# Kernel optimization log

Measured on AMD Instinct MI355X. Metric: run time of the kernel, lower is better.

Reference implementation:

```python
import jax, jax.numpy as jnp
import numpy as np

B, IN_UNITS, C, U, K = 32, 16, 8192, 32, 16
NUM_ITERS = 3


def setup_inputs() -> dict:
    key = jax.random.key(0)
    k1, k2 = jax.random.split(key)
    x = jax.random.normal(k1, (B, IN_UNITS, C), dtype=jnp.float32)
    # W corresponds to the torch parameter of shape (1, C, U, K, IN_UNITS), leading 1 dropped
    W = jax.random.normal(k2, (C, U, K, IN_UNITS), dtype=jnp.float32)
    return {"x": x, "W": W}


def reference(x, W):
    batch = x.shape[0]
    # u_hat[b,c,u,k] = sum_i W[c,u,k,i] * x[b,i,c]   (torch: W @ x after transpose/stack)
    u_hat = jnp.einsum('cuki,bic->bcuk', W, x)
    b_ij = jnp.zeros((C, U), dtype=x.dtype)
    v = None
    for _ in range(NUM_ITERS):
        c_ij = jax.nn.softmax(b_ij, axis=0)            # softmax over in_channels (dim=1 in torch)
        s = jnp.einsum('cu,bcuk->buk', c_ij, u_hat)    # weighted sum over channels
        # squash: note the original sums over dim=2 of (B,1,U,K,1) == the num_units axis
        mag_sq = jnp.sum(s ** 2, axis=1, keepdims=True)  # (B,1,K)
        mag = jnp.sqrt(mag_sq)
        v = mag_sq / (1.0 + mag_sq) * (s / mag)          # (B,U,K)
        # agreement: mean over batch of <u_hat, v>
        a = jnp.einsum('bcuk,buk->cu', u_hat, v) / batch
        b_ij = b_ij + a
    return v[..., None]  # matches torch output (B, num_units, unit_size, 1)
```

## Files before the change

kernel.cpp:

```cpp
#include <hip/hip_runtime.h>

#define CC   8192
#define UU   32
#define KK   16
#define BB   32
#define INU  16
#define UK   512
#define CPB  32
#define NBLK 256

__global__ __launch_bounds__(512, 2) void fused_pass(
    const float* __restrict__ x, const float* __restrict__ W,
    const float* __restrict__ v_in, float* __restrict__ b_io,
    float* __restrict__ S, float* __restrict__ Z)
{
    __shared__ float xs[16 * 516];

    const int t   = threadIdx.x;
    const int bid = blockIdx.x;
    const int c0  = bid * CPB;
    const int u   = t >> 4;
    const int k   = t & 15;

    float v[BB], Sl[BB], uh[BB];
#pragma unroll
    for (int b = 0; b < BB; ++b) { v[b] = v_in[b * UK + t]; Sl[b] = 0.f; }
    float zloc = 0.f;

    float4 w0, w1, w2, w3;
    {
        const float4* p = (const float4*)(W + ((size_t)c0 * UK + t) * INU);
        w0 = p[0]; w1 = p[1]; w2 = p[2]; w3 = p[3];
    }

    for (int cc = 0; cc < CPB; ++cc) {
        if ((cc & 15) == 0) {
            __syncthreads();
            const int cbase = c0 + (cc & ~15);
            for (int j = 0; j < 16; ++j) {
                int idx = j * 512 + t;
                int ccl = idx & 15;
                int bi  = idx >> 4;
                xs[ccl * 516 + bi] = x[bi * CC + cbase + ccl];
            }
            __syncthreads();
        }

        float4 n0, n1, n2, n3;
        const bool have_next = (cc + 1 < CPB);
        if (have_next) {
            const float4* p = (const float4*)(W + ((size_t)(c0 + cc + 1) * UK + t) * INU);
            n0 = p[0]; n1 = p[1]; n2 = p[2]; n3 = p[3];
        }

        const float* xrow = &xs[(cc & 15) * 516];
        float ap = 0.f;
#pragma unroll
        for (int b = 0; b < BB; ++b) {
            const float4* xr = (const float4*)(xrow + b * INU);
            float4 x0 = xr[0], x1 = xr[1], x2 = xr[2], x3 = xr[3];
            float h;
            h = w0.x * x0.x;
            h = fmaf(w0.y, x0.y, h); h = fmaf(w0.z, x0.z, h); h = fmaf(w0.w, x0.w, h);
            h = fmaf(w1.x, x1.x, h); h = fmaf(w1.y, x1.y, h);
            h = fmaf(w1.z, x1.z, h); h = fmaf(w1.w, x1.w, h);
            h = fmaf(w2.x, x2.x, h); h = fmaf(w2.y, x2.y, h);
            h = fmaf(w2.z, x2.z, h); h = fmaf(w2.w, x2.w, h);
            h = fmaf(w3.x, x3.x, h); h = fmaf(w3.y, x3.y, h);
            h = fmaf(w3.z, x3.z, h); h = fmaf(w3.w, x3.w, h);
            uh[b] = h;
            ap = fmaf(h, v[b], ap);
        }

        ap += __shfl_xor(ap, 8);
        ap += __shfl_xor(ap, 4);
        ap += __shfl_xor(ap, 2);
        ap += __shfl_xor(ap, 1);

        const int c = c0 + cc;
        float bnew = b_io[c * UU + u] + ap * (1.0f / (float)BB);
        float e = __expf(bnew);
        zloc += e;
        if (k == 0) b_io[c * UU + u] = bnew;

#pragma unroll
        for (int b = 0; b < BB; ++b) Sl[b] = fmaf(e, uh[b], Sl[b]);

        if (have_next) { w0 = n0; w1 = n1; w2 = n2; w3 = n3; }
    }

#pragma unroll
    for (int b = 0; b < BB; ++b) atomicAdd(S + b * UK + t, Sl[b]);
    if (k == 0) atomicAdd(Z + u, zloc);
}

__global__ void squash_k(const float* __restrict__ S, const float* __restrict__ Z,
                         float* __restrict__ vout)
{
    __shared__ float z_sh[UU];
    __shared__ float s2_sh[UK];
    __shared__ float mag_sh[KK];

    const int b = blockIdx.x;
    const int t = threadIdx.x;

    if (t < UU) z_sh[t] = Z[t];
    float ssum = S[b * UK + t];
    __syncthreads();

    float s = ssum / z_sh[t >> 4];
    s2_sh[t] = s * s;
    __syncthreads();

    if (t < KK) {
        float m = 0.f;
        for (int uu = 0; uu < UU; ++uu) m += s2_sh[uu * KK + t];
        mag_sh[t] = m;
    }
    __syncthreads();

    float msq = mag_sh[t & 15];
    float out = (msq / (1.0f + msq)) * s / sqrtf(msq);
    vout[b * UK + t] = out;
}

extern "C" void kernel_launch(void* const* d_in, const int* in_sizes, int n_in,
                              void* d_out, int out_size, void* d_ws, size_t ws_size,
                              hipStream_t stream)
{
    const float* x = (const float*)d_in[0];
    const float* W = (const float*)d_in[1];
    float* out = (float*)d_out;

    char* ws = (char*)d_ws;
    float* S   = (float*)(ws);
    float* Z   = (float*)(ws + 65536);
    float* vb  = (float*)(ws + 65536 + 256);
    float* bio = (float*)(ws + 65536 + 256 + 65536);

    hipMemsetAsync(vb,  0, BB * UK * 4, stream);
    hipMemsetAsync(bio, 0, CC * UU * 4, stream);

    for (int pass = 0; pass < 3; ++pass) {
        hipMemsetAsync(S, 0, BB * UK * 4, stream);
        hipMemsetAsync(Z, 0, UU * 4, stream);
        fused_pass<<<NBLK, 512, 0, stream>>>(x, W, vb, bio, S, Z);
        float* vo = (pass == 2) ? out : vb;
        squash_k<<<BB, UK, 0, stream>>>(S, Z, vo);
    }
}
```

Measured before the change: 707.1 us.

## Pre-transpose x and stream it through scalar loads instead of LDS staging

Adds a transpose kernel that lays x out as [C][B*IN] so every wave reads the same 16-float row. The main pass then fetches those rows with s_load_dwordx16 into SGPRs, double-buffered, and drops the LDS staging and its barriers. It also halves channels per block to double the grid, raises the occupancy hint, and replaces the per-pass memsets with one upfront memset over per-pass S/Z buffers. The old LDS kernel is kept as a fallback when the workspace is too small. Inline asm waitcnt after every body may serialize latency, and the fallback path adds code.

Measured after the change: 1.006 ms. 1.42x slower.

```diff
diff --git a/kernel.cpp b/kernel.cpp
--- a/kernel.cpp
+++ b/kernel.cpp
@@ -6,16 +6,53 @@
 #define BB   32
 #define INU  16
 #define UK   512
-#define CPB  32
-#define NBLK 256
-
-__global__ __launch_bounds__(512, 2) void fused_pass(
-    const float* __restrict__ x, const float* __restrict__ W,
+#define CPB  16
+#define NBLK 512
+
+typedef __attribute__((ext_vector_type(16))) float f32x16;
+
+__global__ __launch_bounds__(256) void transpose_x(
+    const float* __restrict__ x, float* __restrict__ xT)
+{
+    __shared__ float tile[64][65];
+    const int bc = blockIdx.x & 127;
+    const int bb = blockIdx.x >> 7;
+    const int c0 = bc * 64, bi0 = bb * 64;
+    const int tx = threadIdx.x & 63, ty = threadIdx.x >> 6;
+#pragma unroll
+    for (int j = 0; j < 64; j += 4)
+        tile[ty + j][tx] = x[(size_t)(bi0 + ty + j) * CC + (c0 + tx)];
+    __syncthreads();
+#pragma unroll
+    for (int j = 0; j < 64; j += 4)
+        xT[(size_t)(c0 + ty + j) * (BB * INU) + (bi0 + tx)] = tile[tx][ty + j];
+}
+
+#define SBODY(XC, XN, B, NP)                                                  \
+    asm volatile("s_load_dwordx16 %0, %1, 0" : "=s"(XN) : "s"(NP));           \
+    {                                                                         \
+        float h0 = w0.x * XC[0];                                              \
+        float h1 = w0.z * XC[2];                                              \
+        float h2 = w1.x * XC[4];                                              \
+        float h3 = w1.z * XC[6];                                              \
+        h0 = fmaf(w0.y, XC[1],  h0);  h1 = fmaf(w0.w, XC[3],  h1);            \
+        h2 = fmaf(w1.y, XC[5],  h2);  h3 = fmaf(w1.w, XC[7],  h3);            \
+        h0 = fmaf(w2.x, XC[8],  h0);  h1 = fmaf(w2.z, XC[10], h1);            \
+        h2 = fmaf(w3.x, XC[12], h2);  h3 = fmaf(w3.z, XC[14], h3);            \
+        h0 = fmaf(w2.y, XC[9],  h0);  h1 = fmaf(w2.w, XC[11], h1);            \
+        h2 = fmaf(w3.y, XC[13], h2);  h3 = fmaf(w3.w, XC[15], h3);            \
+        float hs = (h0 + h1) + (h2 + h3);                                     \
+        uh[B] = hs;                                                           \
+        ap = fmaf(hs, v[B], ap);                                              \
+    }                                                                         \
+    asm volatile("s_waitcnt lgkmcnt(0)" : "+s"(XN));                          \
+    __builtin_amdgcn_sched_barrier(0);
+
+__global__ __launch_bounds__(512, 4) void fused_pass(
+    const float* __restrict__ W, const float* __restrict__ xT,
     const float* __restrict__ v_in, float* __restrict__ b_io,
     float* __restrict__ S, float* __restrict__ Z)
 {
-    __shared__ float xs[16 * 516];
-
     const int t   = threadIdx.x;
     const int bid = blockIdx.x;
     const int c0  = bid * CPB;
@@ -33,7 +70,81 @@
         w0 = p[0]; w1 = p[1]; w2 = p[2]; w3 = p[3];
     }
 
+    f32x16 xa, xb;
+    {
+        const float* p0 = xT + (size_t)c0 * (BB * INU);
+        asm volatile("s_load_dwordx16 %0, %1, 0" : "=s"(xa) : "s"(p0));
+        asm volatile("s_waitcnt lgkmcnt(0)" : "+s"(xa));
+        __builtin_amdgcn_sched_barrier(0);
+    }
+
     for (int cc = 0; cc < CPB; ++cc) {
+        float4 n0, n1, n2, n3;
+        const bool have_next = (cc + 1 < CPB);
+        if (have_next) {
+            const float4* p = (const float4*)(W + ((size_t)(c0 + cc + 1) * UK + t) * INU);
+            n0 = p[0]; n1 = p[1]; n2 = p[2]; n3 = p[3];
+        }
+
+        const float* xrow  = xT + (size_t)(c0 + cc) * (BB * INU);
+        const float* xnext = have_next ? (xrow + BB * INU) : xrow;
+
+        float ap = 0.f;
+#pragma unroll
+        for (int b = 0; b < BB; b += 2) {
+            const float* np0 = xrow + (size_t)(b + 1) * INU;
+            SBODY(xa, xb, b, np0)
+            const float* np1 = (b + 2 < BB) ? (xrow + (size_t)(b + 2) * INU) : xnext;
+            SBODY(xb, xa, b + 1, np1)
+        }
+
+        ap += __shfl_xor(ap, 8);
+        ap += __shfl_xor(ap, 4);
+        ap += __shfl_xor(ap, 2);
+        ap += __shfl_xor(ap, 1);
+
+        const int c = c0 + cc;
+        float bnew = b_io[c * UU + u] + ap * (1.0f / (float)BB);
+        float e = __expf(bnew);
+        zloc += e;
+        if (k == 0) b_io[c * UU + u] = bnew;
+
+#pragma unroll
+        for (int b = 0; b < BB; ++b) Sl[b] = fmaf(e, uh[b], Sl[b]);
+
+        if (have_next) { w0 = n0; w1 = n1; w2 = n2; w3 = n3; }
+    }
+
+#pragma unroll
+    for (int b = 0; b < BB; ++b) atomicAdd(S + b * UK + t, Sl[b]);
+    if (k == 0) atomicAdd(Z + u, zloc);
+}
+
+__global__ __launch_bounds__(512, 2) void fused_pass_lds(
+    const float* __restrict__ x, const float* __restrict__ W,
+    const float* __restrict__ v_in, float* __restrict__ b_io,
+    float* __restrict__ S, float* __restrict__ Z)
+{
+    __shared__ float xs[16 * 516];
+
+    const int t   = threadIdx.x;
+    const int bid = blockIdx.x;
+    const int c0  = bid * 32;
+    const int u   = t >> 4;
+    const int k   = t & 15;
+
+    float v[BB], Sl[BB], uh[BB];
+#pragma unroll
+    for (int b = 0; b < BB; ++b) { v[b] = v_in[b * UK + t]; Sl[b] = 0.f; }
+    float zloc = 0.f;
+
+    float4 w0, w1, w2, w3;
+    {
+        const float4* p = (const float4*)(W + ((size_t)c0 * UK + t) * INU);
+        w0 = p[0]; w1 = p[1]; w2 = p[2]; w3 = p[3];
+    }
+
+    for (int cc = 0; cc < 32; ++cc) {
         if ((cc & 15) == 0) {
             __syncthreads();
             const int cbase = c0 + (cc & ~15);
@@ -47,7 +158,7 @@
         }
 
         float4 n0, n1, n2, n3;
-        const bool have_next = (cc + 1 < CPB);
+        const bool have_next = (cc + 1 < 32);
         if (have_next) {
             const float4* p = (const float4*)(W + ((size_t)(c0 + cc + 1) * UK + t) * INU);
             n0 = p[0]; n1 = p[1]; n2 = p[2]; n3 = p[3];
@@ -133,19 +244,42 @@
     float* out = (float*)d_out;
 
     char* ws = (char*)d_ws;
-    float* S   = (float*)(ws);
-    float* Z   = (float*)(ws + 65536);
-    float* vb  = (float*)(ws + 65536 + 256);
-    float* bio = (float*)(ws + 65536 + 256 + 65536);
-
-    hipMemsetAsync(vb,  0, BB * UK * 4, stream);
-    hipMemsetAsync(bio, 0, CC * UU * 4, stream);
-
-    for (int pass = 0; pass < 3; ++pass) {
-        hipMemsetAsync(S, 0, BB * UK * 4, stream);
-        hipMemsetAsync(Z, 0, UU * 4, stream);
-        fused_pass<<<NBLK, 512, 0, stream>>>(x, W, vb, bio, S, Z);
-        float* vo = (pass == 2) ? out : vb;
-        squash_k<<<BB, UK, 0, stream>>>(S, Z, vo);
-    }
-}
+
+    const size_t XT_OFF = 0x140400;
+    const size_t NEED   = XT_OFF + (size_t)CC * BB * INU * 4;
+
+    if (ws_size >= NEED) {
+        float* S3  = (float*)(ws);
+        float* Z3  = (float*)(ws + 0x30000);
+        float* vb  = (float*)(ws + 0x30200);
+        float* bio = (float*)(ws + 0x40200);
+        float* xT  = (float*)(ws + XT_OFF);
+
+        hipMemsetAsync(ws, 0, 0x140200, stream);
+        transpose_x<<<1024, 256, 0, stream>>>(x, xT);
+
+        for (int pass = 0; pass < 3; ++pass) {
+            float* S = S3 + (size_t)pass * (BB * UK);
+            float* Z =3 > 0 ? (Z3 + (size_t)pass * 32) : Z3;
+            fused_pass<<<NBLK, 512, 0, stream>>>(W, xT, vb, bio, S, Z);
+            float* vo = (pass == 2) ? out : vb;
+            squash_k<<<BB, UK, 0, stream>>>(S, Z, vo);
+        }
+    } else {
+        float* S   = (float*)(ws);
+        float* Z   = (float*)(ws + 65536);
+        float* vb  = (float*)(ws + 65536 + 256);
+        float* bio = (float*)(ws + 65536 + 256 + 65536);
+
+        hipMemsetAsync(vb,  0, BB * UK * 4, stream);
+        hipMemsetAsync(bio, 0, CC * UU * 4, stream);
+
+        for (int pass = 0; pass < 3; ++pass) {
+            hipMemsetAsync(S, 0, BB * UK * 4, stream);
+            hipMemsetAsync(Z, 0, UU * 4, stream);
+            fused_pass_lds<<<256, 512, 0, stream>>>(x, W, vb, bio, S, Z);
+            float* vo = (pass == 2) ? out : vb;
+            squash_k<<<BB, UK, 0, stream>>>(S, Z, vo);
+        }
+    }
+}
```

## Compute u_hat with split-bf16 MFMA and pre-transposed x

Applied to the files above, without the earlier changes.

Adds a transpose kernel that lays x out as (C, B*IN) once, then replaces the scalar FMA u_hat computation with bf16 MFMA 16x16x32 instructions. Each fp32 value is split into high and low bf16 parts so three products approximate fp32 accuracy. Per-pass S/Z buffers are zeroed with one memset up front to cut launch overhead. The MFMA path drops the LDS staging of x and uses wave-wide shuffle reductions; the old path is kept as a fallback when the workspace is too small.

New measurement: 811.8 us. 1.15x slower.

```diff
diff --git a/kernel.cpp b/kernel.cpp
--- a/kernel.cpp
+++ b/kernel.cpp
@@ -9,7 +9,186 @@
 #define CPB  32
 #define NBLK 256
 
-__global__ __launch_bounds__(512, 2) void fused_pass(
+typedef __attribute__((ext_vector_type(4))) float  f32x4;
+typedef __attribute__((ext_vector_type(8))) __bf16 bf16x8;
+
+__global__ __launch_bounds__(256) void transpose_x(
+    const float* __restrict__ x, float* __restrict__ xT)
+{
+    __shared__ float tile[64][65];
+    const int bc = blockIdx.x & 127;
+    const int bb = blockIdx.x >> 7;
+    const int c0 = bc * 64, bi0 = bb * 64;
+    const int tx = threadIdx.x & 63, ty = threadIdx.x >> 6;
+#pragma unroll
+    for (int j = 0; j < 64; j += 4)
+        tile[ty + j][tx] = x[(size_t)(bi0 + ty + j) * CC + (c0 + tx)];
+    __syncthreads();
+#pragma unroll
+    for (int j = 0; j < 64; j += 4)
+        xT[(size_t)(c0 + ty + j) * (BB * INU) + (bi0 + tx)] = tile[tx][ty + j];
+}
+
+__device__ inline void split4(f32x4 f, __bf16 h[4], __bf16 l[4])
+{
+#pragma unroll
+    for (int i = 0; i < 4; ++i) {
+        __bf16 hh = (__bf16)f[i];
+        h[i] = hh;
+        l[i] = (__bf16)(f[i] - (float)hh);
+    }
+}
+
+__device__ inline bf16x8 pack8(const __bf16 a[4], const __bf16 b[4])
+{
+    bf16x8 r;
+    r[0] = a[0]; r[1] = a[1]; r[2] = a[2]; r[3] = a[3];
+    r[4] = b[0]; r[5] = b[1]; r[6] = b[2]; r[7] = b[3];
+    return r;
+}
+
+__global__ __launch_bounds__(512, 2) void fused_mfma(
+    const float* __restrict__ W, const float* __restrict__ xT,
+    const float* __restrict__ v_in, float* __restrict__ b_io,
+    float* __restrict__ S, float* __restrict__ Z)
+{
+    const int tid  = threadIdx.x;
+    const int w    = tid >> 6;
+    const int lane = tid & 63;
+    const int col  = lane & 15;
+    const int g    = lane >> 4;
+    const int c0   = blockIdx.x * CPB;
+    const int u0   = w * 4;
+    const int loff = col * 16 + g * 4;
+
+    f32x4 vf[4][2], Sl[4][2];
+#pragma unroll
+    for (int uu = 0; uu < 4; ++uu)
+#pragma unroll
+        for (int bt = 0; bt < 2; ++bt) {
+            const int b = bt * 16 + col;
+#pragma unroll
+            for (int r = 0; r < 4; ++r) {
+                vf[uu][bt][r] = v_in[(size_t)b * UK + (u0 + uu) * KK + g * 4 + r];
+                Sl[uu][bt][r] = 0.f;
+            }
+        }
+    float zl[4] = {0.f, 0.f, 0.f, 0.f};
+
+    f32x4 wf[4], xf[2], bio;
+    {
+        const float* wb = W + ((size_t)c0 * UU + u0) * (KK * INU) + loff;
+#pragma unroll
+        for (int uu = 0; uu < 4; ++uu) wf[uu] = *(const f32x4*)(wb + uu * 256);
+        const float* xb = xT + (size_t)c0 * (BB * INU) + loff;
+        xf[0] = *(const f32x4*)(xb);
+        xf[1] = *(const f32x4*)(xb + 256);
+        bio   = *(const f32x4*)(b_io + (size_t)c0 * UU + u0);
+    }
+
+    const __bf16 zb = (__bf16)0.f;
+    const __bf16 z4[4] = {zb, zb, zb, zb};
+
+    for (int cc = 0; cc < CPB; ++cc) {
+        const int c = c0 + cc;
+        const bool have_next = (cc + 1 < CPB);
+
+        f32x4 wn[4], xn[2], bion;
+        if (have_next) {
+            const float* wb = W + ((size_t)(c + 1) * UU + u0) * (KK * INU) + loff;
+#pragma unroll
+            for (int uu = 0; uu < 4; ++uu) wn[uu] = *(const f32x4*)(wb + uu * 256);
+            const float* xb = xT + (size_t)(c + 1) * (BB * INU) + loff;
+            xn[0] = *(const f32x4*)(xb);
+            xn[1] = *(const f32x4*)(xb + 256);
+            bion  = *(const f32x4*)(b_io + (size_t)(c + 1) * UU + u0);
+        }
+
+        bf16x8 B1[2], B2[2];
+#pragma unroll
+        for (int bt = 0; bt < 2; ++bt) {
+            __bf16 xh[4], xl[4];
+            split4(xf[bt], xh, xl);
+            B1[bt] = pack8(xh, xh);
+            B2[bt] = pack8(xh, xl);
+        }
+
+        f32x4 acc[4][2];
+#pragma unroll
+        for (int uu = 0; uu < 4; ++uu) {
+            __bf16 wh[4], wl[4];
+            split4(wf[uu], wh, wl);
+            bf16x8 A1 = pack8(wh, wl);
+            bf16x8 A2 = pack8(z4, wh);
+#pragma unroll
+            for (int bt = 0; bt < 2; ++bt) {
+                f32x4 t = {0.f, 0.f, 0.f, 0.f};
+                t = __builtin_amdgcn_mfma_f32_16x16x32_bf16(A1, B1[bt], t, 0, 0, 0);
+                t = __builtin_amdgcn_mfma_f32_16x16x32_bf16(A2, B2[bt], t, 0, 0, 0);
+                acc[uu][bt] = t;
+            }
+        }
+
+        float p[4];
+#pragma unroll
+        for (int uu = 0; uu < 4; ++uu) {
+            float d = 0.f;
+#pragma unroll
+            for (int bt = 0; bt < 2; ++bt)
+#pragma unroll
+                for (int r = 0; r < 4; ++r)
+                    d = fmaf(acc[uu][bt][r], vf[uu][bt][r], d);
+            p[uu] = d;
+        }
+#pragma unroll
+        for (int off = 1; off < 64; off <<= 1) {
+            p[0] += __shfl_xor(p[0], off);
+            p[1] += __shfl_xor(p[1], off);
+            p[2] += __shfl_xor(p[2], off);
+            p[3] += __shfl_xor(p[3], off);
+        }
+
+        f32x4 bnew;
+        float e[4];
+#pragma unroll
+        for (int uu = 0; uu < 4; ++uu) {
+            bnew[uu] = bio[uu] + p[uu] * (1.0f / (float)BB);
+            e[uu]    = __expf(bnew[uu]);
+            zl[uu]  += e[uu];
+        }
+        if (lane == 0) *(f32x4*)(b_io + (size_t)c * UU + u0) = bnew;
+
+#pragma unroll
+        for (int uu = 0; uu < 4; ++uu)
+#pragma unroll
+            for (int bt = 0; bt < 2; ++bt)
+#pragma unroll
+                for (int r = 0; r < 4; ++r)
+                    Sl[uu][bt][r] = fmaf(e[uu], acc[uu][bt][r], Sl[uu][bt][r]);
+
+        if (have_next) {
+            wf[0] = wn[0]; wf[1] = wn[1]; wf[2] = wn[2]; wf[3] = wn[3];
+            xf[0] = xn[0]; xf[1] = xn[1];
+            bio   = bion;
+        }
+    }
+
+#pragma unroll
+    for (int uu = 0; uu < 4; ++uu)
+#pragma unroll
+        for (int bt = 0; bt < 2; ++bt) {
+            const int b = bt * 16 + col;
+#pragma unroll
+            for (int r = 0; r < 4; ++r)
+                atomicAdd(S + (size_t)b * UK + (u0 + uu) * KK + g * 4 + r, Sl[uu][bt][r]);
+        }
+    if (lane == 0) {
+#pragma unroll
+        for (int uu = 0; uu < 4; ++uu) atomicAdd(Z + u0 + uu, zl[uu]);
+    }
+}
+
+__global__ __launch_bounds__(512, 2) void fused_pass_lds(
     const float* __restrict__ x, const float* __restrict__ W,
     const float* __restrict__ v_in, float* __restrict__ b_io,
     float* __restrict__ S, float* __restrict__ Z)
@@ -18,7 +197,7 @@
 
     const int t   = threadIdx.x;
     const int bid = blockIdx.x;
-    const int c0  = bid * CPB;
+    const int c0  = bid * 32;
     const int u   = t >> 4;
     const int k   = t & 15;
 
@@ -33,7 +212,7 @@
         w0 = p[0]; w1 = p[1]; w2 = p[2]; w3 = p[3];
     }
 
-    for (int cc = 0; cc < CPB; ++cc) {
+    for (int cc = 0; cc < 32; ++cc) {
         if ((cc & 15) == 0) {
             __syncthreads();
             const int cbase = c0 + (cc & ~15);
@@ -47,7 +226,7 @@
         }
 
         float4 n0, n1, n2, n3;
-        const bool have_next = (cc + 1 < CPB);
+        const bool have_next = (cc + 1 < 32);
         if (have_next) {
             const float4* p = (const float4*)(W + ((size_t)(c0 + cc + 1) * UK + t) * INU);
             n0 = p[0]; n1 = p[1]; n2 = p[2]; n3 = p[3];
@@ -133,19 +312,42 @@
     float* out = (float*)d_out;
 
     char* ws = (char*)d_ws;
-    float* S   = (float*)(ws);
-    float* Z   = (float*)(ws + 65536);
-    float* vb  = (float*)(ws + 65536 + 256);
-    float* bio = (float*)(ws + 65536 + 256 + 65536);
-
-    hipMemsetAsync(vb,  0, BB * UK * 4, stream);
-    hipMemsetAsync(bio, 0, CC * UU * 4, stream);
-
-    for (int pass = 0; pass < 3; ++pass) {
-        hipMemsetAsync(S, 0, BB * UK * 4, stream);
-        hipMemsetAsync(Z, 0, UU * 4, stream);
-        fused_pass<<<NBLK, 512, 0, stream>>>(x, W, vb, bio, S, Z);
-        float* vo = (pass == 2) ? out : vb;
-        squash_k<<<BB, UK, 0, stream>>>(S, Z, vo);
-    }
-}
+
+    const size_t XT_OFF = 0x140400;
+    const size_t NEED   = XT_OFF + (size_t)CC * BB * INU * 4;
+
+    if (ws_size >= NEED) {
+        float* S3  = (float*)(ws);
+        float* Z3  = (float*)(ws + 0x30000);
+        float* vb  = (float*)(ws + 0x30200);
+        float* bio = (float*)(ws + 0x40200);
+        float* xT  = (float*)(ws + XT_OFF);
+
+        hipMemsetAsync(ws, 0, 0x140200, stream);
+        transpose_x<<<1024, 256, 0, stream>>>(x, xT);
+
+        for (int pass = 0; pass < 3; ++pass) {
+            float* S = S3 + (size_t)pass * (BB * UK);
+            float* Z = Z3 + (size_t)pass * 32;
+            fused_mfma<<<NBLK, 512, 0, stream>>>(W, xT, vb, bio, S, Z);
+            float* vo = (pass == 2) ? out : vb;
+            squash_k<<<BB, UK, 0, stream>>>(S, Z, vo);
+        }
+    } else {
+        float* S   = (float*)(ws);
+        float* Z   = (float*)(ws + 65536);
+        float* vb  = (float*)(ws + 65536 + 256);
+        float* bio = (float*)(ws + 65536 + 256 + 65536);
+
+        hipMemsetAsync(vb,  0, BB * UK * 4, stream);
+        hipMemsetAsync(bio, 0, CC * UU * 4, stream);
+
+        for (int pass = 0; pass < 3; ++pass) {
+            hipMemsetAsync(S, 0, BB * UK * 4, stream);
+            hipMemsetAsync(Z, 0, UU * 4, stream);
+            fused_pass_lds<<<256, 512, 0, stream>>>(x, W, vb, bio, S, Z);
+            float* vo = (pass == 2) ? out : vb;
+            squash_k<<<BB, UK, 0, stream>>>(S, Z, vo);
+        }
+    }
+}
```
